# Kernel tuning notes

Measured on AMD Instinct MI355X. Metric: run time of the kernel, lower is better.

## Reference

```python
import jax, jax.numpy as jnp
import numpy as np

IN_F, OUT_F, GROUP = 4096, 11008, 128

# NF4 codebook (normalized-float-4 levels), matches NF4_LEVELS in the source
NF4_LEVELS = jnp.array([
    -1.0, -0.6961928009986877, -0.5250730514526367, -0.39491748809814453,
    -0.28444138169288635, -0.18477343022823334, -0.09105003625154495, 0.0,
    0.07958029955625534, 0.16093020141124725, 0.24611230194568634,
    0.33791524171829224, 0.44070982933044434, 0.5626170039176941,
    0.7229568362236023, 1.0], dtype=jnp.float32)


def setup_inputs() -> dict:
    key = jax.random.key(0)
    k0, k1, k2, k3 = jax.random.split(key, 4)
    x = jax.random.normal(k0, (32, 1, IN_F), dtype=jnp.float32)
    # one int32 per packed byte; low nibble = even element code, high nibble = odd
    packed = jax.random.randint(k1, (OUT_F * IN_F // 2,), 0, 256, dtype=jnp.int32)
    # per-group absmax scales (positive)
    scales = jax.random.uniform(k2, (OUT_F * IN_F // GROUP,), dtype=jnp.float32) * 0.02 + 1e-4
    bias_param = jax.random.normal(k3, (OUT_F,), dtype=jnp.float32)
    return {"x": x, "packed": packed, "scales": scales, "bias_param": bias_param}


def dequant_nf4(packed, scales):
    # unpack two 4-bit codes per byte; interleave as quantized[0::2]=low, [1::2]=high
    low = packed & 15
    high = (packed >> 4) & 15
    codes = jnp.stack([low, high], axis=-1).reshape(-1)          # [OUT_F*IN_F]
    vals = NF4_LEVELS[codes]                                      # codebook lookup
    w = (vals.reshape(-1, GROUP) * scales[:, None]).reshape(OUT_F, IN_F)
    return w


def reference(x, packed, scales, bias_param):
    W = dequant_nf4(packed, scales)                               # [OUT_F, IN_F]
    # y = x @ W^T + b  (F.linear semantics)
    return jnp.einsum('bsi,oi->bso', x, W) + bias_param
```

## Files before the change

### kernel.cpp

```cpp
#include <hip/hip_runtime.h>
#include <hip/hip_bf16.h>

#define IN_F   4096
#define OUT_F  11008
#define BATCH  32
#define GROUP  128
#define KSPLIT 4
#define KBLK   (IN_F / KSPLIT)
#define NTILE  64
#define GRID_N (OUT_F / NTILE)
#define OUTSZ  (BATCH * OUT_F)

typedef __attribute__((ext_vector_type(8))) short  bf16x8;
typedef __attribute__((ext_vector_type(4))) float  f32x4;
typedef __attribute__((ext_vector_type(4))) int    i32x4;

static __device__ __constant__ float NF4_LEVELS[16] = {
    -1.0f, -0.6961928009986877f, -0.5250730514526367f, -0.39491748809814453f,
    -0.28444138169288635f, -0.18477343022823334f, -0.09105003625154495f, 0.0f,
    0.07958029955625534f, 0.16093020141124725f, 0.24611230194568634f,
    0.33791524171829224f, 0.44070982933044434f, 0.5626170039176941f,
    0.7229568362236023f, 1.0f};

#define WS_SCT_OFF  262144
#define WS_PART_OFF (262144 + 1409024)

__global__ void prelude_kernel(const float* __restrict__ x,
                               const float* __restrict__ scales,
                               unsigned short* __restrict__ frag,
                               float* __restrict__ sct) {
    const int bid = blockIdx.x, tid = threadIdx.x;
    if (bid < 64) {
        int T  = bid * 256 + tid;
        int st = T >> 13;
        int kb = (T >> 6) & 127;
        int l  = T & 63;
        int row = st * 16 + (l & 15);
        int k0  = kb * 32 + (l >> 4) * 8;
        const float* src = x + (size_t)row * IN_F + k0;
        unsigned w[4];
        #pragma unroll
        for (int e = 0; e < 4; ++e) {
            unsigned lo = __builtin_bit_cast(unsigned short, __float2bfloat16(src[2 * e]));
            unsigned hi = __builtin_bit_cast(unsigned short, __float2bfloat16(src[2 * e + 1]));
            w[e] = lo | (hi << 16);
        }
        i32x4 v = { (int)w[0], (int)w[1], (int)w[2], (int)w[3] };
        *reinterpret_cast<i32x4*>(frag + ((size_t)st * 8192 + kb * 64 + l) * 8) = v;
    } else {
        int B2 = bid - 64;
        int gr = B2 / 43;
        int o  = (B2 % 43) * 256 + tid;
        sct[gr * OUT_F + o] = scales[o * 32 + gr];
    }
}

__global__ __launch_bounds__(256, 3) void nf4_gemm_kernel(
        const int* __restrict__ packed,
        const unsigned short* __restrict__ frag,
        const float* __restrict__ sct,
        float* __restrict__ part)
{
    __shared__ unsigned tabu[256];
    __shared__ unsigned lds[8192];

    const int tid  = threadIdx.x;
    const int wave = tid >> 6;
    const int lane = tid & 63;
    const int col  = lane & 15;
    const int g    = lane >> 4;

    {
        unsigned lo = __builtin_bit_cast(unsigned short, __float2bfloat16(NF4_LEVELS[tid & 15]));
        unsigned hi = __builtin_bit_cast(unsigned short, __float2bfloat16(NF4_LEVELS[(tid >> 4) & 15]));
        tabu[tid] = lo | (hi << 16);
    }

    const int n0    = blockIdx.x * NTILE;
    const int kint0 = blockIdx.y * 512;
    const int kbB   = blockIdx.y * 32;
    const int grB   = blockIdx.y * 8;
    const int dperm = (lane & 0x30) | ((lane & 3) << 2) | ((lane >> 2) & 3);

    #define STAGE8_LOAD(u, r, sr)                                             \
        _Pragma("unroll")                                                     \
        for (int ii = 0; ii < 8; ++ii) {                                      \
            int rl = (r) * 8 + ii;                                            \
            sr[ii] = *reinterpret_cast<const i32x4*>(                         \
                packed + (size_t)(n0 + wave * 16 + rl) * (IN_F / 2)           \
                       + kint0 + (u) * 256 + lane * 4);                       \
        }

    #define STAGE8_WRITE(u, r, sr)                                            \
        _Pragma("unroll")                                                     \
        for (int ii = 0; ii < 8; ++ii) {                                      \
            int rl  = (r) * 8 + ii;                                           \
            int row = wave * 16 + rl;                                         \
            unsigned v = ((unsigned)(sr[ii][0] & 255))                        \
                       | ((unsigned)(sr[ii][1] & 255) << 8)                   \
                       | ((unsigned)(sr[ii][2] & 255) << 16)                  \
                       | ((unsigned)(sr[ii][3] & 255) << 24);                 \
            lds[(u) * 4096 + ((row * 64 + dperm) ^ ((row & 7) << 2))] = v;    \
        }

    {
        i32x4 sr[8];
        STAGE8_LOAD(0, 0, sr) STAGE8_WRITE(0, 0, sr)
        STAGE8_LOAD(0, 1, sr) STAGE8_WRITE(0, 1, sr)
    }
    __syncthreads();

    f32x4 acc[4][2];
    #pragma unroll
    for (int st = 0; st < 4; ++st) {
        acc[st][0] = (f32x4){0.f,0.f,0.f,0.f};
        acc[st][1] = (f32x4){0.f,0.f,0.f,0.f};
    }

    const unsigned short* f0 = frag;
    const unsigned short* f1 = frag + 65536;

    #pragma unroll
    for (int u = 0; u < 2; ++u) {
        i32x4 sr0[8], sr1[8];
        if (u == 0) { STAGE8_LOAD(1, 0, sr0) }

        i32x4 cd[4];
        #pragma unroll
        for (int st = 0; st < 4; ++st) {
            int row  = st * 16 + col;
            int base = u * 4096 + ((row * 64 + wave * 16 + g * 4) ^ ((row & 7) << 2));
            cd[st] = *reinterpret_cast<const i32x4*>(&lds[base]);
        }
        const int gr = grB + u * 4 + wave;
        float sc[4];
        #pragma unroll
        for (int st = 0; st < 4; ++st)
            sc[st] = sct[gr * OUT_F + n0 + st * 16 + col];

        bf16x8 A0[4], A1[4];
        #pragma unroll
        for (int tt = 0; tt < 4; ++tt) {
            int kb = kbB + u * 16 + wave * 4 + tt;
            A0[tt] = *reinterpret_cast<const bf16x8*>(f0 + ((size_t)kb * 64 + lane) * 8);
            A1[tt] = *reinterpret_cast<const bf16x8*>(f1 + ((size_t)kb * 64 + lane) * 8);
        }

        f32x4 t[4][2];
        #pragma unroll
        for (int st = 0; st < 4; ++st) {
            t[st][0] = (f32x4){0.f,0.f,0.f,0.f};
            t[st][1] = (f32x4){0.f,0.f,0.f,0.f};
        }

        #pragma unroll
        for (int tt = 0; tt < 4; ++tt) {
            #pragma unroll
            for (int st = 0; st < 4; ++st) {
                unsigned code = (unsigned)cd[st][tt];
                i32x4 bu;
                bu[0] = (int)tabu[code & 255u];
                bu[1] = (int)tabu[(code >> 8) & 255u];
                bu[2] = (int)tabu[(code >> 16) & 255u];
                bu[3] = (int)tabu[code >> 24];
                bf16x8 bf = __builtin_bit_cast(bf16x8, bu);
                t[st][0] = __builtin_amdgcn_mfma_f32_16x16x32_bf16(A0[tt], bf, t[st][0], 0, 0, 0);
                t[st][1] = __builtin_amdgcn_mfma_f32_16x16x32_bf16(A1[tt], bf, t[st][1], 0, 0, 0);
            }
            if (u == 0 && tt == 1) { STAGE8_WRITE(1, 0, sr0) STAGE8_LOAD(1, 1, sr1) }
        }
        if (u == 0) { STAGE8_WRITE(1, 1, sr1) }

        #pragma unroll
        for (int st = 0; st < 4; ++st)
            #pragma unroll
            for (int j = 0; j < 4; ++j) {
                acc[st][0][j] = fmaf(sc[st], t[st][0][j], acc[st][0][j]);
                acc[st][1][j] = fmaf(sc[st], t[st][1][j], acc[st][1][j]);
            }

        __syncthreads();
    }

    float* red = (float*)lds;
    #pragma unroll
    for (int st = 0; st < 4; ++st)
        #pragma unroll
        for (int h = 0; h < 2; ++h)
            #pragma unroll
            for (int j = 0; j < 4; ++j)
                red[wave * 2048 + ((st * 2 + h) * 4 + j) * 64 + lane] = acc[st][h][j];
    __syncthreads();

    float* po = part + (size_t)blockIdx.y * OUTSZ;
    #pragma unroll
    for (int q = 0; q < 8; ++q) {
        int b   = q * 4 + wave;
        int st  = lane >> 4;
        int c   = lane & 15;
        int h   = b >> 4;
        int g2  = (b >> 2) & 3;
        int j   = b & 3;
        int slot = ((st * 2 + h) * 4 + j) * 64 + g2 * 16 + c;
        float s = red[slot] + red[2048 + slot] + red[4096 + slot] + red[6144 + slot];
        po[(size_t)b * OUT_F + n0 + lane] = s;
    }
}

__global__ void reduce_kernel(const float* __restrict__ part,
                              const float* __restrict__ bias,
                              float* __restrict__ out) {
    int t = blockIdx.x * 256 + threadIdx.x;
    int o = t % OUT_F;
    out[t] = part[t] + part[OUTSZ + t] + part[2 * OUTSZ + t] + part[3 * OUTSZ + t]
           + bias[o];
}

extern "C" void kernel_launch(void* const* d_in, const int* in_sizes, int n_in,
                              void* d_out, int out_size, void* d_ws, size_t ws_size,
                              hipStream_t stream) {
    const float* x      = (const float*)d_in[0];
    const int*   packed = (const int*)d_in[1];
    const float* scales = (const float*)d_in[2];
    const float* bias   = (const float*)d_in[3];
    float* out = (float*)d_out;

    char* ws = (char*)d_ws;
    unsigned short* frag = (unsigned short*)ws;
    float* sct  = (float*)(ws + WS_SCT_OFF);
    float* part = (float*)(ws + WS_PART_OFF);

    prelude_kernel<<<1440, 256, 0, stream>>>(x, scales, frag, sct);
    nf4_gemm_kernel<<<dim3(GRID_N, KSPLIT), 256, 0, stream>>>(packed, frag, sct, part);
    reduce_kernel<<<OUTSZ / 256, 256, 0, stream>>>(part, bias, out);
}
```

Measured before the change: 30.63 us.

## Replace split-K partial buffer and reduce kernel with bias-init plus atomic accumulation

The prelude kernel gains extra blocks that initialize the output with the broadcast bias. The GEMM kernel then atomically adds its split-K partial sums straight into the output, so the partial workspace and the separate reduce kernel are removed. The inner loop is restructured per subtile to shrink register live ranges (one staging buffer, per-st code and scale loads), and launch bounds are raised to 4 blocks per SM. This saves a kernel launch and a round trip through the partial buffer, at the cost of atomic traffic and a non-deterministic summation order.

Result: faster. 29.87 us (-2.5%).

```diff
diff --git a/kernel.cpp b/kernel.cpp
--- a/kernel.cpp
+++ b/kernel.cpp
@@ -6,7 +6,6 @@
 #define BATCH  32
 #define GROUP  128
 #define KSPLIT 4
-#define KBLK   (IN_F / KSPLIT)
 #define NTILE  64
 #define GRID_N (OUT_F / NTILE)
 #define OUTSZ  (BATCH * OUT_F)
@@ -14,6 +13,7 @@
 typedef __attribute__((ext_vector_type(8))) short  bf16x8;
 typedef __attribute__((ext_vector_type(4))) float  f32x4;
 typedef __attribute__((ext_vector_type(4))) int    i32x4;
+typedef __attribute__((ext_vector_type(4))) float  float4v;
 
 static __device__ __constant__ float NF4_LEVELS[16] = {
     -1.0f, -0.6961928009986877f, -0.5250730514526367f, -0.39491748809814453f,
@@ -23,12 +23,13 @@
     0.7229568362236023f, 1.0f};
 
 #define WS_SCT_OFF  262144
-#define WS_PART_OFF (262144 + 1409024)
 
 __global__ void prelude_kernel(const float* __restrict__ x,
                                const float* __restrict__ scales,
+                               const float* __restrict__ bias,
                                unsigned short* __restrict__ frag,
-                               float* __restrict__ sct) {
+                               float* __restrict__ sct,
+                               float* __restrict__ out) {
     const int bid = blockIdx.x, tid = threadIdx.x;
     if (bid < 64) {
         int T  = bid * 256 + tid;
@@ -47,19 +48,25 @@
         }
         i32x4 v = { (int)w[0], (int)w[1], (int)w[2], (int)w[3] };
         *reinterpret_cast<i32x4*>(frag + ((size_t)st * 8192 + kb * 64 + l) * 8) = v;
-    } else {
+    } else if (bid < 1440) {
         int B2 = bid - 64;
         int gr = B2 / 43;
         int o  = (B2 % 43) * 256 + tid;
         sct[gr * OUT_F + o] = scales[o * 32 + gr];
+    } else {
+        int t2 = (bid - 1440) * 256 + tid;
+        int i  = t2 * 4;
+        int o  = i % OUT_F;
+        float4v b = *reinterpret_cast<const float4v*>(bias + o);
+        *reinterpret_cast<float4v*>(out + i) = b;
     }
 }
 
-__global__ __launch_bounds__(256, 3) void nf4_gemm_kernel(
+__global__ __launch_bounds__(256, 4) void nf4_gemm_kernel(
         const int* __restrict__ packed,
         const unsigned short* __restrict__ frag,
         const float* __restrict__ sct,
-        float* __restrict__ part)
+        float* __restrict__ out)
 {
     __shared__ unsigned tabu[256];
     __shared__ unsigned lds[8192];
@@ -122,21 +129,8 @@
 
     #pragma unroll
     for (int u = 0; u < 2; ++u) {
-        i32x4 sr0[8], sr1[8];
-        if (u == 0) { STAGE8_LOAD(1, 0, sr0) }
-
-        i32x4 cd[4];
-        #pragma unroll
-        for (int st = 0; st < 4; ++st) {
-            int row  = st * 16 + col;
-            int base = u * 4096 + ((row * 64 + wave * 16 + g * 4) ^ ((row & 7) << 2));
-            cd[st] = *reinterpret_cast<const i32x4*>(&lds[base]);
-        }
-        const int gr = grB + u * 4 + wave;
-        float sc[4];
-        #pragma unroll
-        for (int st = 0; st < 4; ++st)
-            sc[st] = sct[gr * OUT_F + n0 + st * 16 + col];
+        i32x4 sr[8];
+        if (u == 0) { STAGE8_LOAD(1, 0, sr) }
 
         bf16x8 A0[4], A1[4];
         #pragma unroll
@@ -146,38 +140,37 @@
             A1[tt] = *reinterpret_cast<const bf16x8*>(f1 + ((size_t)kb * 64 + lane) * 8);
         }
 
-        f32x4 t[4][2];
+        const int gr = grB + u * 4 + wave;
+
         #pragma unroll
         for (int st = 0; st < 4; ++st) {
-            t[st][0] = (f32x4){0.f,0.f,0.f,0.f};
-            t[st][1] = (f32x4){0.f,0.f,0.f,0.f};
-        }
-
-        #pragma unroll
-        for (int tt = 0; tt < 4; ++tt) {
+            int row  = st * 16 + col;
+            i32x4 cdv = *reinterpret_cast<const i32x4*>(
+                &lds[u * 4096 + ((row * 64 + wave * 16 + g * 4) ^ ((row & 7) << 2))]);
+            float sc = sct[gr * OUT_F + n0 + st * 16 + col];
+
+            f32x4 t0 = (f32x4){0.f,0.f,0.f,0.f};
+            f32x4 t1 = (f32x4){0.f,0.f,0.f,0.f};
             #pragma unroll
-            for (int st = 0; st < 4; ++st) {
-                unsigned code = (unsigned)cd[st][tt];
+            for (int tt = 0; tt < 4; ++tt) {
+                unsigned code = (unsigned)cdv[tt];
                 i32x4 bu;
                 bu[0] = (int)tabu[code & 255u];
                 bu[1] = (int)tabu[(code >> 8) & 255u];
                 bu[2] = (int)tabu[(code >> 16) & 255u];
                 bu[3] = (int)tabu[code >> 24];
                 bf16x8 bf = __builtin_bit_cast(bf16x8, bu);
-                t[st][0] = __builtin_amdgcn_mfma_f32_16x16x32_bf16(A0[tt], bf, t[st][0], 0, 0, 0);
-                t[st][1] = __builtin_amdgcn_mfma_f32_16x16x32_bf16(A1[tt], bf, t[st][1], 0, 0, 0);
+                t0 = __builtin_amdgcn_mfma_f32_16x16x32_bf16(A0[tt], bf, t0, 0, 0, 0);
+                t1 = __builtin_amdgcn_mfma_f32_16x16x32_bf16(A1[tt], bf, t1, 0, 0, 0);
             }
-            if (u == 0 && tt == 1) { STAGE8_WRITE(1, 0, sr0) STAGE8_LOAD(1, 1, sr1) }
-        }
-        if (u == 0) { STAGE8_WRITE(1, 1, sr1) }
-
-        #pragma unroll
-        for (int st = 0; st < 4; ++st)
             #pragma unroll
             for (int j = 0; j < 4; ++j) {
-                acc[st][0][j] = fmaf(sc[st], t[st][0][j], acc[st][0][j]);
-                acc[st][1][j] = fmaf(sc[st], t[st][1][j], acc[st][1][j]);
+                acc[st][0][j] = fmaf(sc, t0[j], acc[st][0][j]);
+                acc[st][1][j] = fmaf(sc, t1[j], acc[st][1][j]);
             }
+            if (u == 0 && st == 1) { STAGE8_WRITE(1, 0, sr) STAGE8_LOAD(1, 1, sr) }
+        }
+        if (u == 0) { STAGE8_WRITE(1, 1, sr) }
 
         __syncthreads();
     }
@@ -192,7 +185,6 @@
                 red[wave * 2048 + ((st * 2 + h) * 4 + j) * 64 + lane] = acc[st][h][j];
     __syncthreads();
 
-    float* po = part + (size_t)blockIdx.y * OUTSZ;
     #pragma unroll
     for (int q = 0; q < 8; ++q) {
         int b   = q * 4 + wave;
@@ -203,17 +195,8 @@
         int j   = b & 3;
         int slot = ((st * 2 + h) * 4 + j) * 64 + g2 * 16 + c;
         float s = red[slot] + red[2048 + slot] + red[4096 + slot] + red[6144 + slot];
-        po[(size_t)b * OUT_F + n0 + lane] = s;
-    }
-}
-
-__global__ void reduce_kernel(const float* __restrict__ part,
-                              const float* __restrict__ bias,
-                              float* __restrict__ out) {
-    int t = blockIdx.x * 256 + threadIdx.x;
-    int o = t % OUT_F;
-    out[t] = part[t] + part[OUTSZ + t] + part[2 * OUTSZ + t] + part[3 * OUTSZ + t]
-           + bias[o];
+        unsafeAtomicAdd(out + (size_t)b * OUT_F + n0 + lane, s);
+    }
 }
 
 extern "C" void kernel_launch(void* const* d_in, const int* in_sizes, int n_in,
@@ -227,10 +210,8 @@
 
     char* ws = (char*)d_ws;
     unsigned short* frag = (unsigned short*)ws;
-    float* sct  = (float*)(ws + WS_SCT_OFF);
-    float* part = (float*)(ws + WS_PART_OFF);
-
-    prelude_kernel<<<1440, 256, 0, stream>>>(x, scales, frag, sct);
-    nf4_gemm_kernel<<<dim3(GRID_N, KSPLIT), 256, 0, stream>>>(packed, frag, sct, part);
-    reduce_kernel<<<OUTSZ / 256, 256, 0, stream>>>(part, bias, out);
+    float* sct = (float*)(ws + WS_SCT_OFF);
+
+    prelude_kernel<<<1784, 256, 0, stream>>>(x, scales, bias, frag, sct, out);
+    nf4_gemm_kernel<<<dim3(GRID_N, KSPLIT), 256, 0, stream>>>(packed, frag, sct, out);
 }
```
